# Optimization experiments

Hardware: AMD Instinct MI355X
Metric: run time of the kernel (lower is better)

## Reference

```python
import jax, jax.numpy as jnp
import numpy as np

NUM_OPS, B, T, D = 8, 8, 512, 1024


def setup_inputs() -> dict:
    key = jax.random.key(0)
    k1, k2, k3, k4 = jax.random.split(key, 4)
    x = jax.random.normal(k1, (B, T, D), dtype=jnp.float32)
    W = jax.random.normal(k2, (NUM_OPS, D, D), dtype=jnp.float32) * 0.02
    b = jnp.zeros((NUM_OPS, D), dtype=jnp.float32)
    logits = 0.001 * jax.random.normal(k3, (NUM_OPS,), dtype=jnp.float32)
    # uniform noise for Gumbel sampling (matches tf.random.uniform in sample_without_replacement)
    u = jax.random.uniform(k4, (NUM_OPS,), dtype=jnp.float32, minval=1e-6, maxval=1.0 - 1e-6)
    return {"x": x, "W": W, "b": b, "logits": logits, "u": u}


def reference(x, W, b, logits, u):
    # weights = softmax(logits); gumbel top-1 over log(weights) == log_softmax(logits)
    gumbel = -jnp.log(-jnp.log(u))
    idx = jnp.argmax(jax.nn.log_softmax(logits) + gumbel)
    # forward of ops_times_mask_binary: sum over ON ops (num_on_samples=1 -> single op)
    out = jnp.einsum('btd,de->bte', x, W[idx]) + b[idx]  # [B,T,D]
    return out
```

## Files before the change

kernel.cpp:

```cpp
#include <hip/hip_runtime.h>

typedef unsigned short u16;
typedef __attribute__((ext_vector_type(8))) short bf16x8;
typedef __attribute__((ext_vector_type(4))) float f32x4;

#define NUM_OPS 8
#define M_DIM 4096
#define K_DIM 1024
#define N_DIM 1024


__device__ __forceinline__ u16 f2b(float f) {
  union { float f; unsigned u; } v; v.f = f;
  unsigned r = v.u + 0x7fffu + ((v.u >> 16) & 1u);
  return (u16)(r >> 16);
}

__device__ __forceinline__ int compute_idx(const float* __restrict__ logits,
                                           const float* __restrict__ u) {
  int best = 0; float bv = -3.4e38f;
#pragma unroll
  for (int i = 0; i < NUM_OPS; ++i) {
    float g = -logf(-logf(u[i]));
    float v = logits[i] + g;
    if (v > bv) { bv = v; best = i; }
  }
  return best;
}

__device__ __forceinline__ void gld_lds16(const void* g, void* l) {
  __builtin_amdgcn_global_load_lds(
      (__attribute__((address_space(1))) void*)(g),
      (__attribute__((address_space(3))) void*)(unsigned)(unsigned long long)(l),
      16, 0, 0);
}

__global__ void prep_kernel(const float* __restrict__ x, const float* __restrict__ W,
                            const float* __restrict__ logits, const float* __restrict__ u,
                            u16* __restrict__ xb, u16* __restrict__ wt) {
  const int tid = threadIdx.x;
  const int bid = blockIdx.x;
  if (bid < 2048) {
    size_t i0 = ((size_t)bid * 256 + tid) * 8;
    const float4* xp = (const float4*)(x + i0);
    float4 f0 = xp[0], f1 = xp[1];
    unsigned p0 = (unsigned)f2b(f0.x) | ((unsigned)f2b(f0.y) << 16);
    unsigned p1 = (unsigned)f2b(f0.z) | ((unsigned)f2b(f0.w) << 16);
    unsigned p2 = (unsigned)f2b(f1.x) | ((unsigned)f2b(f1.y) << 16);
    unsigned p3 = (unsigned)f2b(f1.z) | ((unsigned)f2b(f1.w) << 16);
    uint4 pk; pk.x = p0; pk.y = p1; pk.z = p2; pk.w = p3;
    *(uint4*)(xb + i0) = pk;
  } else {
    __shared__ u16 t[64][66];
    const int wb = bid - 2048;
    const int kt = wb >> 4, nt = wb & 15;
    const int idx = compute_idx(logits, u);
    const float* Wi = W + (size_t)idx * K_DIM * N_DIM;
#pragma unroll
    for (int it = 0; it < 16; ++it) {
      int i = it * 256 + tid;
      int r = i >> 6, c = i & 63;
      t[r][c] = f2b(Wi[(size_t)(kt * 64 + r) * N_DIM + nt * 64 + c]);
    }
    __syncthreads();
#pragma unroll
    for (int it = 0; it < 16; ++it) {
      int i = it * 256 + tid;
      int n = i >> 6, k = i & 63;
      wt[(size_t)(nt * 64 + n) * K_DIM + kt * 64 + k] = t[k][n];
    }
  }
}

__global__ __launch_bounds__(256) void gemm_kernel(
    const u16* __restrict__ xb, const u16* __restrict__ wt,
    const float* __restrict__ bvec, const float* __restrict__ logits,
    const float* __restrict__ u, float* __restrict__ out) {
  __shared__ u16 sA[128 * 32];
  __shared__ u16 sB[64 * 32];

  const int tid = threadIdx.x;
  const int w = tid >> 6, L = tid & 63;
  const int m0 = blockIdx.y * 128;
  const int n0 = blockIdx.x * 64;

  const int q0 = 2 * w, q1 = 2 * w + 1;
  const u16* gA0 = xb + (size_t)(m0 + 16 * q0 + (L >> 2)) * K_DIM + (L & 3) * 8;
  const u16* gA1 = xb + (size_t)(m0 + 16 * q1 + (L >> 2)) * K_DIM + (L & 3) * 8;
  const u16* gB0 = wt + (size_t)(n0 + 16 * w + (L >> 2)) * K_DIM + (L & 3) * 8;
  u16* lA0 = sA + q0 * 512 + L * 8;
  u16* lA1 = sA + q1 * 512 + L * 8;
  u16* lB0 = sB + w * 512 + L * 8;

  const int wm = w & 1, wn = w >> 1;
  int aoff[4], boff[2];
#pragma unroll
  for (int mt = 0; mt < 4; ++mt)
    aoff[mt] = (64 * wm + 16 * mt + (L & 15)) * 32 + (L >> 4) * 8;
#pragma unroll
  for (int nt = 0; nt < 2; ++nt)
    boff[nt] = (32 * wn + 16 * nt + (L & 15)) * 32 + (L >> 4) * 8;

  f32x4 acc[4][2] = {};

  for (int kk = 0; kk < K_DIM / 32; ++kk) {
    __syncthreads();
    gld_lds16(gA0, lA0);
    gld_lds16(gA1, lA1);
    gld_lds16(gB0, lB0);
    gA0 += 32; gA1 += 32; gB0 += 32;
    __syncthreads();

    bf16x8 af[4], bf[2];
#pragma unroll
    for (int mt = 0; mt < 4; ++mt) af[mt] = *(const bf16x8*)(sA + aoff[mt]);
#pragma unroll
    for (int nt = 0; nt < 2; ++nt) bf[nt] = *(const bf16x8*)(sB + boff[nt]);
#pragma unroll
    for (int mt = 0; mt < 4; ++mt)
#pragma unroll
      for (int nt = 0; nt < 2; ++nt)
        acc[mt][nt] = __builtin_amdgcn_mfma_f32_16x16x32_bf16(
            af[mt], bf[nt], acc[mt][nt], 0, 0, 0);
  }

  const int idx = compute_idx(logits, u);
  const float* bi = bvec + (size_t)idx * N_DIM;
#pragma unroll
  for (int mt = 0; mt < 4; ++mt) {
    int row = m0 + 64 * wm + 16 * mt + (L >> 4) * 4;
#pragma unroll
    for (int nt = 0; nt < 2; ++nt) {
      int col = n0 + 32 * wn + 16 * nt + (L & 15);
      float bv = bi[col];
#pragma unroll
      for (int r = 0; r < 4; ++r)
        out[(size_t)(row + r) * N_DIM + col] = acc[mt][nt][r] + bv;
    }
  }
}


extern "C" void kernel_launch(void* const* d_in, const int* in_sizes, int n_in,
                              void* d_out, int out_size, void* d_ws, size_t ws_size,
                              hipStream_t stream) {
  const float* x      = (const float*)d_in[0];
  const float* W      = (const float*)d_in[1];
  const float* bvec   = (const float*)d_in[2];
  const float* logits = (const float*)d_in[3];
  const float* u      = (const float*)d_in[4];
  float* out = (float*)d_out;

  u16* xb = (u16*)d_ws;
  u16* wt = (u16*)d_ws + (size_t)M_DIM * K_DIM;

  prep_kernel<<<2048 + 256, 256, 0, stream>>>(x, W, logits, u, xb, wt);
  dim3 grid(N_DIM / 64, M_DIM / 128);
  gemm_kernel<<<grid, 256, 0, stream>>>(xb, wt, bvec, logits, u, out);
}
```

Measured before the change: 112.7 us.

## Double-buffer LDS tiles and enlarge GEMM block tile to 128x128

The GEMM kernel now keeps two LDS buffers for A and B and issues the global-to-LDS loads for the next K step before computing on the current one, with one barrier per iteration instead of two. The N tile per block doubles from 64 to 128, so each wave computes a 64x64 sub-tile with 16 MFMA accumulators, which raises data reuse per loaded tile. The aim is to hide global load latency and reduce barrier and load overhead. In exchange the grid shrinks to 256 blocks and register and LDS use per block rise, which may lower occupancy and leave fewer blocks per CU on a 256-CU part.

```diff
diff --git a/kernel.cpp b/kernel.cpp
--- a/kernel.cpp
+++ b/kernel.cpp
@@ -76,52 +76,63 @@
     const u16* __restrict__ xb, const u16* __restrict__ wt,
     const float* __restrict__ bvec, const float* __restrict__ logits,
     const float* __restrict__ u, float* __restrict__ out) {
-  __shared__ u16 sA[128 * 32];
-  __shared__ u16 sB[64 * 32];
+  __shared__ u16 sA[2][128 * 32];
+  __shared__ u16 sB[2][128 * 32];
 
   const int tid = threadIdx.x;
   const int w = tid >> 6, L = tid & 63;
   const int m0 = blockIdx.y * 128;
-  const int n0 = blockIdx.x * 64;
+  const int n0 = blockIdx.x * 128;
 
   const int q0 = 2 * w, q1 = 2 * w + 1;
-  const u16* gA0 = xb + (size_t)(m0 + 16 * q0 + (L >> 2)) * K_DIM + (L & 3) * 8;
-  const u16* gA1 = xb + (size_t)(m0 + 16 * q1 + (L >> 2)) * K_DIM + (L & 3) * 8;
-  const u16* gB0 = wt + (size_t)(n0 + 16 * w + (L >> 2)) * K_DIM + (L & 3) * 8;
-  u16* lA0 = sA + q0 * 512 + L * 8;
-  u16* lA1 = sA + q1 * 512 + L * 8;
-  u16* lB0 = sB + w * 512 + L * 8;
+  const int rlo = (L >> 2), cofs = (L & 3) * 8;
+  const u16* gA0 = xb + (size_t)(m0 + 16 * q0 + rlo) * K_DIM + cofs;
+  const u16* gA1 = xb + (size_t)(m0 + 16 * q1 + rlo) * K_DIM + cofs;
+  const u16* gB0 = wt + (size_t)(n0 + 16 * q0 + rlo) * K_DIM + cofs;
+  const u16* gB1 = wt + (size_t)(n0 + 16 * q1 + rlo) * K_DIM + cofs;
+  const int lofs0 = q0 * 512 + L * 8;
+  const int lofs1 = q1 * 512 + L * 8;
 
   const int wm = w & 1, wn = w >> 1;
-  int aoff[4], boff[2];
+  int aoff[4], boff[4];
 #pragma unroll
-  for (int mt = 0; mt < 4; ++mt)
-    aoff[mt] = (64 * wm + 16 * mt + (L & 15)) * 32 + (L >> 4) * 8;
-#pragma unroll
-  for (int nt = 0; nt < 2; ++nt)
-    boff[nt] = (32 * wn + 16 * nt + (L & 15)) * 32 + (L >> 4) * 8;
+  for (int t = 0; t < 4; ++t) {
+    aoff[t] = (64 * wm + 16 * t + (L & 15)) * 32 + (L >> 4) * 8;
+    boff[t] = (64 * wn + 16 * t + (L & 15)) * 32 + (L >> 4) * 8;
+  }
 
-  f32x4 acc[4][2] = {};
+  f32x4 acc[4][4] = {};
+
+  gld_lds16(gA0, &sA[0][lofs0]);
+  gld_lds16(gA1, &sA[0][lofs1]);
+  gld_lds16(gB0, &sB[0][lofs0]);
+  gld_lds16(gB1, &sB[0][lofs1]);
+  __syncthreads();
 
   for (int kk = 0; kk < K_DIM / 32; ++kk) {
-    __syncthreads();
-    gld_lds16(gA0, lA0);
-    gld_lds16(gA1, lA1);
-    gld_lds16(gB0, lB0);
-    gA0 += 32; gA1 += 32; gB0 += 32;
-    __syncthreads();
+    const int cur = kk & 1, nxt = cur ^ 1;
+    if (kk + 1 < K_DIM / 32) {
+      const int ko = (kk + 1) * 32;
+      gld_lds16(gA0 + ko, &sA[nxt][lofs0]);
+      gld_lds16(gA1 + ko, &sA[nxt][lofs1]);
+      gld_lds16(gB0 + ko, &sB[nxt][lofs0]);
+      gld_lds16(gB1 + ko, &sB[nxt][lofs1]);
+    }
 
-    bf16x8 af[4], bf[2];
+    bf16x8 af[4], bf[4];
 #pragma unroll
-    for (int mt = 0; mt < 4; ++mt) af[mt] = *(const bf16x8*)(sA + aoff[mt]);
-#pragma unroll
-    for (int nt = 0; nt < 2; ++nt) bf[nt] = *(const bf16x8*)(sB + boff[nt]);
+    for (int t = 0; t < 4; ++t) {
+      af[t] = *(const bf16x8*)(&sA[cur][0] + aoff[t]);
+      bf[t] = *(const bf16x8*)(&sB[cur][0] + boff[t]);
+    }
 #pragma unroll
     for (int mt = 0; mt < 4; ++mt)
 #pragma unroll
-      for (int nt = 0; nt < 2; ++nt)
+      for (int nt = 0; nt < 4; ++nt)
         acc[mt][nt] = __builtin_amdgcn_mfma_f32_16x16x32_bf16(
             af[mt], bf[nt], acc[mt][nt], 0, 0, 0);
+
+    __syncthreads();
   }
 
   const int idx = compute_idx(logits, u);
@@ -130,8 +141,8 @@
   for (int mt = 0; mt < 4; ++mt) {
     int row = m0 + 64 * wm + 16 * mt + (L >> 4) * 4;
 #pragma unroll
-    for (int nt = 0; nt < 2; ++nt) {
-      int col = n0 + 32 * wn + 16 * nt + (L & 15);
+    for (int nt = 0; nt < 4; ++nt) {
+      int col = n0 + 64 * wn + 16 * nt + (L & 15);
       float bv = bi[col];
 #pragma unroll
       for (int r = 0; r < 4; ++r)
@@ -155,6 +166,6 @@
   u16* wt = (u16*)d_ws + (size_t)M_DIM * K_DIM;
 
   prep_kernel<<<2048 + 256, 256, 0, stream>>>(x, W, logits, u, xb, wt);
-  dim3 grid(N_DIM / 64, M_DIM / 128);
+  dim3 grid(N_DIM / 128, M_DIM / 128);
   gemm_kernel<<<grid, 256, 0, stream>>>(xb, wt, bvec, logits, u, out);
 }
```

New measurement: 118.5 us. +5.1%, slower.

## Fuse bf16 conversion into GEMM with register-prefetched double-buffered LDS tiles

Applied to the files above, without the earlier changes.

Drops the separate prep kernel that wrote bf16 copies of x and a transposed W to workspace. The GEMM now reads fp32 x and the selected W directly, converts them to bf16 in registers, and writes them into padded, double-buffered LDS tiles. The next K-slice is prefetched into registers while MFMAs run on the current one, with one barrier per iteration. The block tile grows to 128x128 with 512 threads. This removes the workspace write and re-read and a launch, at the cost of more global traffic per tile (fp32 re-read across blocks, strided W column loads) and round-half-up rounding instead of round-to-nearest-even.

```diff
diff --git a/kernel.cpp b/kernel.cpp
--- a/kernel.cpp
+++ b/kernel.cpp
@@ -1,6 +1,7 @@
 #include <hip/hip_runtime.h>
 
 typedef unsigned short u16;
+typedef unsigned int u32;
 typedef __attribute__((ext_vector_type(8))) short bf16x8;
 typedef __attribute__((ext_vector_type(4))) float f32x4;
 
@@ -8,13 +9,10 @@
 #define M_DIM 4096
 #define K_DIM 1024
 #define N_DIM 1024
+#define BK 32
+#define PITCH 40
+#define KITERS (K_DIM / BK)
 
-
-__device__ __forceinline__ u16 f2b(float f) {
-  union { float f; unsigned u; } v; v.f = f;
-  unsigned r = v.u + 0x7fffu + ((v.u >> 16) & 1u);
-  return (u16)(r >> 16);
-}
 
 __device__ __forceinline__ int compute_idx(const float* __restrict__ logits,
                                            const float* __restrict__ u) {
@@ -28,94 +26,76 @@
   return best;
 }
 
-__device__ __forceinline__ void gld_lds16(const void* g, void* l) {
-  __builtin_amdgcn_global_load_lds(
-      (__attribute__((address_space(1))) void*)(g),
-      (__attribute__((address_space(3))) void*)(unsigned)(unsigned long long)(l),
-      16, 0, 0);
+__device__ __forceinline__ u32 pk2(float a, float b) {
+  u32 ua = __float_as_uint(a) + 0x8000u;
+  u32 ub = __float_as_uint(b) + 0x8000u;
+  return (ua >> 16) | (ub & 0xffff0000u);
 }
 
-__global__ void prep_kernel(const float* __restrict__ x, const float* __restrict__ W,
-                            const float* __restrict__ logits, const float* __restrict__ u,
-                            u16* __restrict__ xb, u16* __restrict__ wt) {
-  const int tid = threadIdx.x;
-  const int bid = blockIdx.x;
-  if (bid < 2048) {
-    size_t i0 = ((size_t)bid * 256 + tid) * 8;
-    const float4* xp = (const float4*)(x + i0);
-    float4 f0 = xp[0], f1 = xp[1];
-    unsigned p0 = (unsigned)f2b(f0.x) | ((unsigned)f2b(f0.y) << 16);
-    unsigned p1 = (unsigned)f2b(f0.z) | ((unsigned)f2b(f0.w) << 16);
-    unsigned p2 = (unsigned)f2b(f1.x) | ((unsigned)f2b(f1.y) << 16);
-    unsigned p3 = (unsigned)f2b(f1.z) | ((unsigned)f2b(f1.w) << 16);
-    uint4 pk; pk.x = p0; pk.y = p1; pk.z = p2; pk.w = p3;
-    *(uint4*)(xb + i0) = pk;
-  } else {
-    __shared__ u16 t[64][66];
-    const int wb = bid - 2048;
-    const int kt = wb >> 4, nt = wb & 15;
-    const int idx = compute_idx(logits, u);
-    const float* Wi = W + (size_t)idx * K_DIM * N_DIM;
-#pragma unroll
-    for (int it = 0; it < 16; ++it) {
-      int i = it * 256 + tid;
-      int r = i >> 6, c = i & 63;
-      t[r][c] = f2b(Wi[(size_t)(kt * 64 + r) * N_DIM + nt * 64 + c]);
-    }
-    __syncthreads();
-#pragma unroll
-    for (int it = 0; it < 16; ++it) {
-      int i = it * 256 + tid;
-      int n = i >> 6, k = i & 63;
-      wt[(size_t)(nt * 64 + n) * K_DIM + kt * 64 + k] = t[k][n];
-    }
-  }
-}
-
-__global__ __launch_bounds__(256) void gemm_kernel(
-    const u16* __restrict__ xb, const u16* __restrict__ wt,
+__global__ __launch_bounds__(512) void fused_kernel(
+    const float* __restrict__ x, const float* __restrict__ W,
     const float* __restrict__ bvec, const float* __restrict__ logits,
     const float* __restrict__ u, float* __restrict__ out) {
-  __shared__ u16 sA[128 * 32];
-  __shared__ u16 sB[64 * 32];
+  __shared__ u16 sA[2][128 * PITCH];
+  __shared__ u16 sB[2][128 * PITCH];
 
   const int tid = threadIdx.x;
   const int w = tid >> 6, L = tid & 63;
   const int m0 = blockIdx.y * 128;
-  const int n0 = blockIdx.x * 64;
+  const int n0 = blockIdx.x * 128;
 
-  const int q0 = 2 * w, q1 = 2 * w + 1;
-  const u16* gA0 = xb + (size_t)(m0 + 16 * q0 + (L >> 2)) * K_DIM + (L & 3) * 8;
-  const u16* gA1 = xb + (size_t)(m0 + 16 * q1 + (L >> 2)) * K_DIM + (L & 3) * 8;
-  const u16* gB0 = wt + (size_t)(n0 + 16 * w + (L >> 2)) * K_DIM + (L & 3) * 8;
-  u16* lA0 = sA + q0 * 512 + L * 8;
-  u16* lA1 = sA + q1 * 512 + L * 8;
-  u16* lB0 = sB + w * 512 + L * 8;
+  const int idx = compute_idx(logits, u);
+  const float* Wi = W + (size_t)idx * K_DIM * N_DIM;
+
+  const int am = tid >> 2, akq = tid & 3;
+  const float* gA = x + (size_t)(m0 + am) * K_DIM + akq * 8;
+  const int lA = am * PITCH + akq * 8;
+
+  const int bn = tid & 127, bkg = tid >> 7;
+  const float* gB = Wi + (size_t)(bkg * 8) * N_DIM + n0 + bn;
+  const int lB = bn * PITCH + bkg * 8;
 
   const int wm = w & 1, wn = w >> 1;
   int aoff[4], boff[2];
 #pragma unroll
   for (int mt = 0; mt < 4; ++mt)
-    aoff[mt] = (64 * wm + 16 * mt + (L & 15)) * 32 + (L >> 4) * 8;
+    aoff[mt] = (64 * wm + 16 * mt + (L & 15)) * PITCH + (L >> 4) * 8;
 #pragma unroll
   for (int nt = 0; nt < 2; ++nt)
-    boff[nt] = (32 * wn + 16 * nt + (L & 15)) * 32 + (L >> 4) * 8;
+    boff[nt] = (32 * wn + 16 * nt + (L & 15)) * PITCH + (L >> 4) * 8;
 
   f32x4 acc[4][2] = {};
 
-  for (int kk = 0; kk < K_DIM / 32; ++kk) {
+  float4 ra0 = *(const float4*)(gA);
+  float4 ra1 = *(const float4*)(gA + 4);
+  float rb[8];
+#pragma unroll
+  for (int j = 0; j < 8; ++j) rb[j] = gB[(size_t)j * N_DIM];
+
+  for (int kk = 0; kk < KITERS; ++kk) {
+    const int cur = kk & 1;
+    uint4 pa; pa.x = pk2(ra0.x, ra0.y); pa.y = pk2(ra0.z, ra0.w);
+    pa.z = pk2(ra1.x, ra1.y); pa.w = pk2(ra1.z, ra1.w);
+    *(uint4*)(&sA[cur][lA]) = pa;
+    uint4 pb; pb.x = pk2(rb[0], rb[1]); pb.y = pk2(rb[2], rb[3]);
+    pb.z = pk2(rb[4], rb[5]); pb.w = pk2(rb[6], rb[7]);
+    *(uint4*)(&sB[cur][lB]) = pb;
     __syncthreads();
-    gld_lds16(gA0, lA0);
-    gld_lds16(gA1, lA1);
-    gld_lds16(gB0, lB0);
-    gA0 += 32; gA1 += 32; gB0 += 32;
-    __syncthreads();
+
+    if (kk + 1 < KITERS) {
+      const float* gA2 = gA + (kk + 1) * BK;
+      ra0 = *(const float4*)(gA2);
+      ra1 = *(const float4*)(gA2 + 4);
+      const float* gB2 = gB + (size_t)(kk + 1) * BK * N_DIM;
+#pragma unroll
+      for (int j = 0; j < 8; ++j) rb[j] = gB2[(size_t)j * N_DIM];
+    }
 
     bf16x8 af[4], bf[2];
 #pragma unroll
-    for (int mt = 0; mt < 4; ++mt) af[mt] = *(const bf16x8*)(sA + aoff[mt]);
+    for (int mt = 0; mt < 4; ++mt) af[mt] = *(const bf16x8*)(&sA[cur][aoff[mt]]);
 #pragma unroll
-    for (int nt = 0; nt < 2; ++nt) bf[nt] = *(const bf16x8*)(sB + boff[nt]);
+    for (int nt = 0; nt < 2; ++nt) bf[nt] = *(const bf16x8*)(&sB[cur][boff[nt]]);
 #pragma unroll
     for (int mt = 0; mt < 4; ++mt)
 #pragma unroll
@@ -124,7 +104,6 @@
             af[mt], bf[nt], acc[mt][nt], 0, 0, 0);
   }
 
-  const int idx = compute_idx(logits, u);
   const float* bi = bvec + (size_t)idx * N_DIM;
 #pragma unroll
   for (int mt = 0; mt < 4; ++mt) {
@@ -151,10 +130,6 @@
   const float* u      = (const float*)d_in[4];
   float* out = (float*)d_out;
 
-  u16* xb = (u16*)d_ws;
-  u16* wt = (u16*)d_ws + (size_t)M_DIM * K_DIM;
-
-  prep_kernel<<<2048 + 256, 256, 0, stream>>>(x, W, logits, u, xb, wt);
-  dim3 grid(N_DIM / 64, M_DIM / 128);
-  gemm_kernel<<<grid, 256, 0, stream>>>(xb, wt, bvec, logits, u, out);
+  dim3 grid(N_DIM / 128, M_DIM / 128);
+  fused_kernel<<<grid, 512, 0, stream>>>(x, W, bvec, logits, u, out);
 }
```

After: 120.0 us. 1.06x slower.
